# Performance work log

Hardware: AMD Instinct MI355X
Metric: run time of the kernel (lower is better)

## Reference

```python
import jax, jax.numpy as jnp
import numpy as np

NEG_INF = -1e9  # matches masked_fill value -1000000000.0
LEAKY_SLOPE = 0.2


def setup_inputs() -> dict:
    key = jax.random.key(0)
    k1, k2, k3, k4 = jax.random.split(key, 4)
    B, N, D_in, D_out = 8, 2048, 256, 256
    x = jax.random.normal(k1, (B, N, D_in), dtype=jnp.float32)
    adj_matrix = jax.random.randint(k2, (B, N, N), 0, 2, dtype=jnp.int32)
    # torch nn.Linear weights: W is [out, in], attention a is [1, 2*out]
    W = jax.random.normal(k3, (D_out, D_in), dtype=jnp.float32) / np.sqrt(D_in)
    a = jax.random.normal(k4, (1, 2 * D_out), dtype=jnp.float32) / np.sqrt(2 * D_out)
    return {"x": x, "adj_matrix": adj_matrix, "W": W, "a": a}


def reference(x, adj_matrix, W, a):
    # h = W(x): [B, N, D_out]
    h = jnp.einsum('bnd,od->bno', x, W)
    D = h.shape[-1]
    # attention(concat(h_i, h_j)) == h_i @ a_left + h_j @ a_right (bias-free linear)
    a_left, a_right = a[0, :D], a[0, D:]
    e = (h @ a_left)[:, :, None] + (h @ a_right)[:, None, :]  # [B, N, N]
    e = jnp.where(e > 0, e, LEAKY_SLOPE * e)  # LeakyReLU(0.2)
    e = jnp.where(adj_matrix == 0, NEG_INF, e)
    alpha = jax.nn.softmax(e, axis=-1)
    return jnp.einsum('bij,bjd->bid', alpha, h)
```

## Files before the change

kernel.cpp:

```cpp
#include <hip/hip_runtime.h>
#include <hip/hip_bf16.h>

typedef __attribute__((ext_vector_type(8))) __bf16 bf16x8;
typedef __attribute__((ext_vector_type(4))) float f32x4;
typedef __attribute__((ext_vector_type(4))) int int4v;

#define NB 8
#define NN 2048
#define ND 256
#define L2E 1.44269504f

__global__ __launch_bounds__(256) void k2_elr(
    const float* __restrict__ x, const float* __restrict__ W,
    const float* __restrict__ a, float* __restrict__ elc,
    float* __restrict__ er2) {
  __shared__ float wls[ND], wrs[ND];
  int t = threadIdx.x;
  {
    float swl = 0.f, swr = 0.f;
    for (int o = 0; o < ND; ++o) {
      float wv = W[(long)o * ND + t];
      swl = fmaf(a[o], wv, swl);
      swr = fmaf(a[ND + o], wv, swr);
    }
    wls[t] = swl;
    wrs[t] = swr;
  }
  __syncthreads();
  int r = t >> 2, q = t & 3;
  long row = (long)blockIdx.x * 64 + r;
  const f32x4* xr = (const f32x4*)(x + row * ND);
  float sl = 0.f, sr = 0.f;
#pragma unroll
  for (int ii = 0; ii < 16; ++ii) {
    int idx = q + (ii << 2);
    f32x4 xv = xr[idx];
    f32x4 lv = *(const f32x4*)(wls + idx * 4);
    f32x4 rv = *(const f32x4*)(wrs + idx * 4);
    sl += xv[0] * lv[0] + xv[1] * lv[1] + xv[2] * lv[2] + xv[3] * lv[3];
    sr += xv[0] * rv[0] + xv[1] * rv[1] + xv[2] * rv[2] + xv[3] * rv[3];
  }
  sl += __shfl_xor(sl, 1);
  sl += __shfl_xor(sl, 2);
  sr += __shfl_xor(sr, 1);
  sr += __shfl_xor(sr, 2);
  if (q == 0) {
    elc[row] = (-0.8f * sl - 16.0f) * L2E;
    float2 v;
    v.x = (sr - 16.0f) * L2E;
    v.y = 0.2f * sr * L2E;
    *(float2*)(er2 + row * 2) = v;
  }
}

__global__ __launch_bounds__(256) void k1_h(
    const float* __restrict__ x, const float* __restrict__ W,
    __bf16* __restrict__ hT) {
  __shared__ __bf16 hlds[256 * 34];
  int tid = threadIdx.x;
  int wid = tid >> 6, lane = tid & 63;
  int msub = wid & 1, nh = wid >> 1;
  int lrow = lane & 15, kg = lane >> 4;
  int m0 = blockIdx.x * 32;
  int row = m0 + msub * 16 + lrow;

  f32x4 acc[8];
#pragma unroll
  for (int f = 0; f < 8; ++f) acc[f] = (f32x4){0.f, 0.f, 0.f, 0.f};

#pragma unroll
  for (int k0 = 0; k0 < ND; k0 += 32) {
    int kk = k0 + kg * 8;
    const f32x4* xa = (const f32x4*)(x + (long)row * ND + kk);
    f32x4 a0 = xa[0], a1 = xa[1];
    bf16x8 afrag;
    afrag[0] = (__bf16)a0[0]; afrag[1] = (__bf16)a0[1];
    afrag[2] = (__bf16)a0[2]; afrag[3] = (__bf16)a0[3];
    afrag[4] = (__bf16)a1[0]; afrag[5] = (__bf16)a1[1];
    afrag[6] = (__bf16)a1[2]; afrag[7] = (__bf16)a1[3];
#pragma unroll
    for (int f = 0; f < 8; ++f) {
      int o = nh * 128 + f * 16 + lrow;
      const f32x4* wb = (const f32x4*)(W + (long)o * ND + kk);
      f32x4 b0 = wb[0], b1 = wb[1];
      bf16x8 bfrag;
      bfrag[0] = (__bf16)b0[0]; bfrag[1] = (__bf16)b0[1];
      bfrag[2] = (__bf16)b0[2]; bfrag[3] = (__bf16)b0[3];
      bfrag[4] = (__bf16)b1[0]; bfrag[5] = (__bf16)b1[1];
      bfrag[6] = (__bf16)b1[2]; bfrag[7] = (__bf16)b1[3];
      acc[f] = __builtin_amdgcn_mfma_f32_16x16x32_bf16(afrag, bfrag, acc[f], 0, 0, 0);
    }
  }

#pragma unroll
  for (int f = 0; f < 8; ++f) {
    int d = nh * 128 + f * 16 + lrow;
#pragma unroll
    for (int r = 0; r < 4; ++r) {
      int nloc = msub * 16 + kg * 4 + r;
      hlds[d * 34 + nloc] = (__bf16)acc[f][r];
    }
  }
  __syncthreads();
  {
    int b = m0 >> 11;
    int n0 = m0 & (NN - 1);
    const int* src = (const int*)(hlds + tid * 34);
    int tmp[16];
#pragma unroll
    for (int j = 0; j < 16; ++j) tmp[j] = src[j];
    __bf16* dst = hT + ((long)b * ND + tid) * NN + n0;
#pragma unroll
    for (int j = 0; j < 4; ++j)
      *(int4v*)(dst + j * 8) = *(int4v*)(tmp + j * 4);
  }
}

__global__ __launch_bounds__(256, 2) void k3_main(
    const int* __restrict__ adj, const __bf16* __restrict__ hT,
    const float* __restrict__ elc, const float* __restrict__ er2,
    float* __restrict__ out) {
  __shared__ __bf16 hbuf[3][256 * 32];

  int blk = blockIdx.x;
  int b = blk & 7;
  int it = blk >> 3;
  int tid = threadIdx.x;
  int wid = tid >> 6, lane = tid & 63;
  int isub = wid & 1, dh = wid >> 1;
  int lrow = lane & 15, kg = lane >> 4;
  int irow = it * 32 + isub * 16 + lrow;

  const __bf16* hTb = hT + (long)b * ND * NN;
  const int* adjrow = adj + ((long)b * NN + irow) * NN;
  const float* er2b = er2 + (long)b * NN * 2;
  float c1s = elc[b * NN + irow];
  int kg8 = kg * 8;

  int d0 = tid >> 2;
  int spp = tid & 3;
  int jlog = (spp ^ ((d0 >> 1) & 3)) * 8;
  const __bf16* sbase = hTb + (long)d0 * NN + jlog;

  int sp_r = kg ^ ((lrow >> 1) & 3);
  int hoff = (dh * 128 + lrow) * 64 + sp_r * 16;
  int d_base = dh * 128 + lrow;

  f32x4 acc[8];
#pragma unroll
  for (int f = 0; f < 8; ++f) acc[f] = (f32x4){0.f, 0.f, 0.f, 0.f};
  float den = 0.f;

  int4v aj0_0, aj1_0, aj0_1, aj1_1, aj0_2, aj1_2;
  f32x4 e0_0, e1_0, e2_0, e3_0;
  f32x4 e0_1, e1_1, e2_1, e3_1;
  f32x4 e0_2, e1_2, e2_2, e3_2;

#define STAGEH(BI, TCV)                                                       \
  {                                                                           \
    const __bf16* s0 = sbase + (TCV)*32;                                      \
    _Pragma("unroll") for (int rr = 0; rr < 4; ++rr) {                        \
      __builtin_amdgcn_global_load_lds(                                       \
          (const __attribute__((address_space(1))) void*)(s0 + (long)rr * 64 * NN), \
          (__attribute__((address_space(3))) void*)(&hbuf[BI][0] +            \
                                                    (rr * 256 + tid) * 8),    \
          16, 0, 0);                                                          \
    }                                                                         \
  }

#define LOADSET(S, TCV)                                                       \
  {                                                                           \
    const int* ap = adjrow + (TCV)*32 + kg8;                                  \
    aj0_##S = *(const int4v*)(ap);                                            \
    aj1_##S = *(const int4v*)(ap + 4);                                        \
    const float* ep = er2b + ((TCV)*32 + kg8) * 2;                            \
    e0_##S = *(const f32x4*)(ep);                                             \
    e1_##S = *(const f32x4*)(ep + 4);                                         \
    e2_##S = *(const f32x4*)(ep + 8);                                         \
    e3_##S = *(const f32x4*)(ep + 12);                                        \
  }

#define COMPUTE(BI, S)                                                        \
  {                                                                           \
    bf16x8 pfrag;                                                             \
    float ps = 0.f;                                                           \
    _Pragma("unroll") for (int e = 0; e < 8; ++e) {                           \
      f32x4 ev = (e < 2) ? e0_##S : (e < 4) ? e1_##S : (e < 6) ? e2_##S : e3_##S; \
      float x16 = ev[(e & 1) * 2];                                            \
      float x02 = ev[(e & 1) * 2 + 1];                                        \
      int aj = (e < 4) ? aj0_##S[e] : aj1_##S[e & 3];                         \
      float m = fmaxf(x16, x02 + c1s);                                        \
      float p = __builtin_amdgcn_exp2f(m);                                    \
      p = aj ? p : 0.0f;                                                      \
      ps += p;                                                                \
      pfrag[e] = (__bf16)p;                                                   \
    }                                                                         \
    den += ps;                                                                \
    const char* hb = (const char*)&hbuf[BI][0];                               \
    __builtin_amdgcn_s_setprio(1);                                            \
    _Pragma("unroll") for (int f = 0; f < 8; ++f) {                           \
      bf16x8 bfr = *(const bf16x8*)(hb + hoff + f * 1024);                    \
      acc[f] = __builtin_amdgcn_mfma_f32_16x16x32_bf16(pfrag, bfr, acc[f], 0, 0, 0); \
    }                                                                         \
    __builtin_amdgcn_s_setprio(0);                                            \
  }

#define WAITB(VMN)                                            \
  asm volatile("s_waitcnt vmcnt(" VMN ")" ::: "memory");      \
  __builtin_amdgcn_s_barrier();

  LOADSET(0, 0);
  STAGEH(0, 0);
  LOADSET(1, 1);
  STAGEH(1, 1);

  for (int t3 = 0; t3 < 20; ++t3) {
    int tc = t3 * 3;
    WAITB("10");
    STAGEH(2, tc + 2);
    LOADSET(2, tc + 2);
    COMPUTE(0, 0);
    WAITB("10");
    STAGEH(0, tc + 3);
    LOADSET(0, tc + 3);
    COMPUTE(1, 1);
    WAITB("10");
    STAGEH(1, tc + 4);
    LOADSET(1, tc + 4);
    COMPUTE(2, 2);
  }
  WAITB("10");
  STAGEH(2, 62);
  LOADSET(2, 62);
  COMPUTE(0, 0);
  WAITB("10");
  STAGEH(0, 63);
  LOADSET(0, 63);
  COMPUTE(1, 1);
  WAITB("10");
  COMPUTE(2, 2);
  WAITB("0");
  COMPUTE(0, 0);

#undef STAGEH
#undef LOADSET
#undef COMPUTE
#undef WAITB

  den += __shfl_xor(den, 16);
  den += __shfl_xor(den, 32);
  float rdiv[4];
#pragma unroll
  for (int r = 0; r < 4; ++r) rdiv[r] = 1.0f / __shfl(den, kg * 4 + r);

  float* outb = out + ((long)b * NN + it * 32 + isub * 16) * ND;
#pragma unroll
  for (int f = 0; f < 8; ++f) {
    int dcol = d_base + f * 16;
#pragma unroll
    for (int r = 0; r < 4; ++r)
      outb[(long)(kg * 4 + r) * ND + dcol] = acc[f][r] * rdiv[r];
  }
}

extern "C" void kernel_launch(void* const* d_in, const int* in_sizes, int n_in,
                              void* d_out, int out_size, void* d_ws,
                              size_t ws_size, hipStream_t stream) {
  const float* x = (const float*)d_in[0];
  const int* adj = (const int*)d_in[1];
  const float* W = (const float*)d_in[2];
  const float* a = (const float*)d_in[3];
  float* out = (float*)d_out;

  char* ws = (char*)d_ws;
  const size_t base = 8u * 1024u * 1024u;
  __bf16* hT = (__bf16*)ws;
  float* elc = (float*)(ws + base);
  float* er2 = (float*)(ws + base + 65536u);

  k1_h<<<dim3(512), dim3(256), 0, stream>>>(x, W, hT);
  k2_elr<<<dim3(256), dim3(256), 0, stream>>>(x, W, a, elc, er2);
  k3_main<<<dim3(512), dim3(256), 0, stream>>>(adj, hT, elc, er2, out);
}
```

Before: 127.2 us.

## Retile attention-aggregation kernel: chunked h layout, 512 threads, 4-stage pipeline, LDS er

The h projection is now written in a chunk-contiguous [b][j-chunk][d][32] layout, so each 32-column stage of h is one contiguous 16 KB block staged with two global_load_lds per thread. The main kernel doubles to 512 threads, so each wave owns 64 output columns instead of 128 and halves its accumulator registers. The ring buffer grows from three to four stages. The per-column er terms are preloaded once into LDS instead of being re-read from global memory on every stage. The aim is more latency hiding and less redundant global traffic, at the cost of about 80 KB of LDS per block, which may limit how many blocks fit per CU.

```diff
diff --git a/kernel.cpp b/kernel.cpp
--- a/kernel.cpp
+++ b/kernel.cpp
@@ -9,6 +9,8 @@
 #define NN 2048
 #define ND 256
 #define L2E 1.44269504f
+#define AS1 __attribute__((address_space(1)))
+#define AS3 __attribute__((address_space(3)))
 
 __global__ __launch_bounds__(256) void k2_elr(
     const float* __restrict__ x, const float* __restrict__ W,
@@ -55,7 +57,7 @@
 
 __global__ __launch_bounds__(256) void k1_h(
     const float* __restrict__ x, const float* __restrict__ W,
-    __bf16* __restrict__ hT) {
+    __bf16* __restrict__ hT2) {
   __shared__ __bf16 hlds[256 * 34];
   int tid = threadIdx.x;
   int wid = tid >> 6, lane = tid & 63;
@@ -104,23 +106,24 @@
   __syncthreads();
   {
     int b = m0 >> 11;
-    int n0 = m0 & (NN - 1);
+    int jc = (m0 & (NN - 1)) >> 5;
     const int* src = (const int*)(hlds + tid * 34);
     int tmp[16];
 #pragma unroll
     for (int j = 0; j < 16; ++j) tmp[j] = src[j];
-    __bf16* dst = hT + ((long)b * ND + tid) * NN + n0;
+    __bf16* dst = hT2 + (((long)b * 64 + jc) * 256 + tid) * 32;
 #pragma unroll
     for (int j = 0; j < 4; ++j)
       *(int4v*)(dst + j * 8) = *(int4v*)(tmp + j * 4);
   }
 }
 
-__global__ __launch_bounds__(256, 2) void k3_main(
-    const int* __restrict__ adj, const __bf16* __restrict__ hT,
+__global__ __launch_bounds__(512, 4) void k3_main(
+    const int* __restrict__ adj, const __bf16* __restrict__ hT2,
     const float* __restrict__ elc, const float* __restrict__ er2,
     float* __restrict__ out) {
-  __shared__ __bf16 hbuf[3][256 * 32];
+  __shared__ __bf16 hbuf[4][8192];
+  __shared__ float er_lds[NN * 2];
 
   int blk = blockIdx.x;
   int b = blk & 7;
@@ -131,119 +134,101 @@
   int lrow = lane & 15, kg = lane >> 4;
   int irow = it * 32 + isub * 16 + lrow;
 
-  const __bf16* hTb = hT + (long)b * ND * NN;
+  const __bf16* hT2b = hT2 + (long)b * 64 * 8192;
   const int* adjrow = adj + ((long)b * NN + irow) * NN;
   const float* er2b = er2 + (long)b * NN * 2;
   float c1s = elc[b * NN + irow];
   int kg8 = kg * 8;
 
-  int d0 = tid >> 2;
-  int spp = tid & 3;
-  int jlog = (spp ^ ((d0 >> 1) & 3)) * 8;
-  const __bf16* sbase = hTb + (long)d0 * NN + jlog;
-
-  int sp_r = kg ^ ((lrow >> 1) & 3);
-  int hoff = (dh * 128 + lrow) * 64 + sp_r * 16;
-  int d_base = dh * 128 + lrow;
-
-  f32x4 acc[8];
-#pragma unroll
-  for (int f = 0; f < 8; ++f) acc[f] = (f32x4){0.f, 0.f, 0.f, 0.f};
+  __builtin_amdgcn_global_load_lds((const AS1 void*)(er2b + tid * 4),
+                                   (AS3 void*)(er_lds + tid * 4), 16, 0, 0);
+  __builtin_amdgcn_global_load_lds((const AS1 void*)(er2b + 2048 + tid * 4),
+                                   (AS3 void*)(er_lds + 2048 + tid * 4), 16, 0, 0);
+
+  int d0 = tid >> 2, slot = tid & 3;
+  int jlog = slot ^ (d0 & 3) ^ ((d0 >> 2) & 3);
+  const __bf16* sgbase = hT2b + d0 * 32 + jlog * 8;
+
+  int slot_r = kg ^ (lrow & 3) ^ ((lrow >> 2) & 3);
+  int hoff = (dh * 64 + lrow) * 64 + slot_r * 16;
+  int d_base = dh * 64 + lrow;
+
+  f32x4 acc[4];
+#pragma unroll
+  for (int f = 0; f < 4; ++f) acc[f] = (f32x4){0.f, 0.f, 0.f, 0.f};
   float den = 0.f;
 
-  int4v aj0_0, aj1_0, aj0_1, aj1_1, aj0_2, aj1_2;
-  f32x4 e0_0, e1_0, e2_0, e3_0;
-  f32x4 e0_1, e1_1, e2_1, e3_1;
-  f32x4 e0_2, e1_2, e2_2, e3_2;
-
-#define STAGEH(BI, TCV)                                                       \
-  {                                                                           \
-    const __bf16* s0 = sbase + (TCV)*32;                                      \
-    _Pragma("unroll") for (int rr = 0; rr < 4; ++rr) {                        \
-      __builtin_amdgcn_global_load_lds(                                       \
-          (const __attribute__((address_space(1))) void*)(s0 + (long)rr * 64 * NN), \
-          (__attribute__((address_space(3))) void*)(&hbuf[BI][0] +            \
-                                                    (rr * 256 + tid) * 8),    \
-          16, 0, 0);                                                          \
-    }                                                                         \
-  }
-
-#define LOADSET(S, TCV)                                                       \
-  {                                                                           \
-    const int* ap = adjrow + (TCV)*32 + kg8;                                  \
-    aj0_##S = *(const int4v*)(ap);                                            \
-    aj1_##S = *(const int4v*)(ap + 4);                                        \
-    const float* ep = er2b + ((TCV)*32 + kg8) * 2;                            \
-    e0_##S = *(const f32x4*)(ep);                                             \
-    e1_##S = *(const f32x4*)(ep + 4);                                         \
-    e2_##S = *(const f32x4*)(ep + 8);                                         \
-    e3_##S = *(const f32x4*)(ep + 12);                                        \
-  }
-
-#define COMPUTE(BI, S)                                                        \
-  {                                                                           \
-    bf16x8 pfrag;                                                             \
-    float ps = 0.f;                                                           \
-    _Pragma("unroll") for (int e = 0; e < 8; ++e) {                           \
-      f32x4 ev = (e < 2) ? e0_##S : (e < 4) ? e1_##S : (e < 6) ? e2_##S : e3_##S; \
-      float x16 = ev[(e & 1) * 2];                                            \
-      float x02 = ev[(e & 1) * 2 + 1];                                        \
-      int aj = (e < 4) ? aj0_##S[e] : aj1_##S[e & 3];                         \
-      float m = fmaxf(x16, x02 + c1s);                                        \
-      float p = __builtin_amdgcn_exp2f(m);                                    \
-      p = aj ? p : 0.0f;                                                      \
-      ps += p;                                                                \
-      pfrag[e] = (__bf16)p;                                                   \
-    }                                                                         \
-    den += ps;                                                                \
-    const char* hb = (const char*)&hbuf[BI][0];                               \
-    __builtin_amdgcn_s_setprio(1);                                            \
-    _Pragma("unroll") for (int f = 0; f < 8; ++f) {                           \
-      bf16x8 bfr = *(const bf16x8*)(hb + hoff + f * 1024);                    \
+  int4v aj0_0, aj1_0, aj0_1, aj1_1, aj0_2, aj1_2, aj0_3, aj1_3;
+
+#define STAGEH(BI, TCV)                                                     \
+  {                                                                         \
+    const __bf16* s_ = sgbase + (long)(TCV)*8192;                           \
+    __builtin_amdgcn_global_load_lds((const AS1 void*)(s_),                 \
+                                     (AS3 void*)(&hbuf[BI][tid * 8]), 16, 0, 0); \
+    __builtin_amdgcn_global_load_lds(                                       \
+        (const AS1 void*)(s_ + 4096),                                       \
+        (AS3 void*)(&hbuf[BI][4096 + tid * 8]), 16, 0, 0);                  \
+  }
+
+#define LOADADJ(S, TCV)                                                     \
+  {                                                                         \
+    const int* ap_ = adjrow + (TCV)*32 + kg8;                               \
+    aj0_##S = *(const int4v*)(ap_);                                         \
+    aj1_##S = *(const int4v*)(ap_ + 4);                                     \
+  }
+
+#define COMPUTE(BI, S, TCV)                                                 \
+  {                                                                         \
+    const float* ep_ = er_lds + ((TCV)*32 + kg8) * 2;                       \
+    f32x4 e0 = *(const f32x4*)(ep_);                                        \
+    f32x4 e1 = *(const f32x4*)(ep_ + 4);                                    \
+    f32x4 e2 = *(const f32x4*)(ep_ + 8);                                    \
+    f32x4 e3 = *(const f32x4*)(ep_ + 12);                                   \
+    bf16x8 pfrag;                                                           \
+    float ps = 0.f;                                                         \
+    _Pragma("unroll") for (int e = 0; e < 8; ++e) {                         \
+      f32x4 ev = (e < 2) ? e0 : (e < 4) ? e1 : (e < 6) ? e2 : e3;           \
+      float x16 = ev[(e & 1) * 2];                                          \
+      float x02 = ev[(e & 1) * 2 + 1];                                      \
+      int aj = (e < 4) ? aj0_##S[e] : aj1_##S[e & 3];                       \
+      float m = fmaxf(x16, x02 + c1s);                                      \
+      float p = __builtin_amdgcn_exp2f(m);                                  \
+      p = aj ? p : 0.0f;                                                    \
+      ps += p;                                                              \
+      pfrag[e] = (__bf16)p;                                                 \
+    }                                                                       \
+    den += ps;                                                              \
+    const char* hb = (const char*)&hbuf[BI][0];                             \
+    __builtin_amdgcn_s_setprio(1);                                          \
+    _Pragma("unroll") for (int f = 0; f < 4; ++f) {                         \
+      bf16x8 bfr = *(const bf16x8*)(hb + hoff + f * 1024);                  \
       acc[f] = __builtin_amdgcn_mfma_f32_16x16x32_bf16(pfrag, bfr, acc[f], 0, 0, 0); \
-    }                                                                         \
-    __builtin_amdgcn_s_setprio(0);                                            \
-  }
-
-#define WAITB(VMN)                                            \
-  asm volatile("s_waitcnt vmcnt(" VMN ")" ::: "memory");      \
+    }                                                                       \
+    __builtin_amdgcn_s_setprio(0);                                          \
+  }
+
+#define WAITB(VMN)                                       \
+  asm volatile("s_waitcnt vmcnt(" VMN ")" ::: "memory"); \
   __builtin_amdgcn_s_barrier();
 
-  LOADSET(0, 0);
-  STAGEH(0, 0);
-  LOADSET(1, 1);
-  STAGEH(1, 1);
-
-  for (int t3 = 0; t3 < 20; ++t3) {
-    int tc = t3 * 3;
-    WAITB("10");
-    STAGEH(2, tc + 2);
-    LOADSET(2, tc + 2);
-    COMPUTE(0, 0);
-    WAITB("10");
-    STAGEH(0, tc + 3);
-    LOADSET(0, tc + 3);
-    COMPUTE(1, 1);
-    WAITB("10");
-    STAGEH(1, tc + 4);
-    LOADSET(1, tc + 4);
-    COMPUTE(2, 2);
-  }
-  WAITB("10");
-  STAGEH(2, 62);
-  LOADSET(2, 62);
-  COMPUTE(0, 0);
-  WAITB("10");
-  STAGEH(0, 63);
-  LOADSET(0, 63);
-  COMPUTE(1, 1);
-  WAITB("10");
-  COMPUTE(2, 2);
-  WAITB("0");
-  COMPUTE(0, 0);
+  LOADADJ(0, 0); STAGEH(0, 0);
+  LOADADJ(1, 1); STAGEH(1, 1);
+  LOADADJ(2, 2); STAGEH(2, 2);
+
+  for (int t4 = 0; t4 < 15; ++t4) {
+    int tc = t4 * 4;
+    WAITB("8"); STAGEH(3, tc + 3); LOADADJ(3, tc + 3); COMPUTE(0, 0, tc);
+    WAITB("8"); STAGEH(0, tc + 4); LOADADJ(0, tc + 4); COMPUTE(1, 1, tc + 1);
+    WAITB("8"); STAGEH(1, tc + 5); LOADADJ(1, tc + 5); COMPUTE(2, 2, tc + 2);
+    WAITB("8"); STAGEH(2, tc + 6); LOADADJ(2, tc + 6); COMPUTE(3, 3, tc + 3);
+  }
+  WAITB("8"); STAGEH(3, 63); LOADADJ(3, 63); COMPUTE(0, 0, 60);
+  WAITB("8"); COMPUTE(1, 1, 61);
+  WAITB("4"); COMPUTE(2, 2, 62);
+  WAITB("0"); COMPUTE(3, 3, 63);
 
 #undef STAGEH
-#undef LOADSET
+#undef LOADADJ
 #undef COMPUTE
 #undef WAITB
 
@@ -255,7 +240,7 @@
 
   float* outb = out + ((long)b * NN + it * 32 + isub * 16) * ND;
 #pragma unroll
-  for (int f = 0; f < 8; ++f) {
+  for (int f = 0; f < 4; ++f) {
     int dcol = d_base + f * 16;
 #pragma unroll
     for (int r = 0; r < 4; ++r)
@@ -274,11 +259,11 @@
 
   char* ws = (char*)d_ws;
   const size_t base = 8u * 1024u * 1024u;
-  __bf16* hT = (__bf16*)ws;
+  __bf16* hT2 = (__bf16*)ws;
   float* elc = (float*)(ws + base);
   float* er2 = (float*)(ws + base + 65536u);
 
-  k1_h<<<dim3(512), dim3(256), 0, stream>>>(x, W, hT);
+  k1_h<<<dim3(512), dim3(256), 0, stream>>>(x, W, hT2);
   k2_elr<<<dim3(256), dim3(256), 0, stream>>>(x, W, a, elc, er2);
-  k3_main<<<dim3(512), dim3(256), 0, stream>>>(adj, hT, elc, er2, out);
-}
+  k3_main<<<dim3(512), dim3(512), 0, stream>>>(adj, hT2, elc, er2, out);
+}
```

Result: slower. 131.8 us (+3.7%).
